# Optimization experiments

Measured on AMD Instinct MI355X. Metric: run time of the kernel, lower is better.

## Reference

```python
import jax, jax.numpy as jnp
import numpy as np

V, E, H, T, B = 32000, 1024, 1024, 128, 128


def setup_inputs() -> dict:
    key = jax.random.key(0)
    ks = jax.random.split(key, 12)
    inp = {
        "batch_a": jax.random.randint(ks[0], (T, B), 0, V),
        "batch_b": jax.random.randint(ks[1], (T, B), 0, V),
        "h0_a": jax.random.normal(ks[2], (B, H), jnp.float32),
        "c0_a": jax.random.normal(ks[3], (B, H), jnp.float32),
        "h0_b": jax.random.normal(ks[4], (B, H), jnp.float32),
        "c0_b": jax.random.normal(ks[5], (B, H), jnp.float32),
    }
    # shared encoder parameters (encoder_a and encoder_b are the same weights)
    emb = jax.random.normal(ks[6], (V, E), jnp.float32) * 0.02
    emb = emb.at[0].set(0.0)  # padding_idx=0
    scale = 1.0 / np.sqrt(H)
    inp["emb"] = emb
    inp["w_ih"] = jax.random.uniform(ks[7], (4 * H, E), jnp.float32, -scale, scale)
    inp["w_hh"] = jax.random.uniform(ks[8], (4 * H, H), jnp.float32, -scale, scale)
    b_ih = jax.random.uniform(ks[9], (4 * H,), jnp.float32, -scale, scale)
    b_hh = jax.random.uniform(ks[10], (4 * H,), jnp.float32, -scale, scale)
    # forget-gate bias filled with 2.5 (initialize_parameters fills [H:2H])
    inp["b_ih"] = b_ih.at[H:2 * H].set(2.5)
    inp["b_hh"] = b_hh.at[H:2 * H].set(2.5)
    return inp


def _lstm_final_hidden(ids, h0, c0, emb, w_ih, w_hh, b):
    # ids: [T, B]; returns final hidden state [B, H]
    x_seq = emb[ids]  # [T, B, E]

    def step(carry, x):
        h, c = carry
        gates = x @ w_ih.T + h @ w_hh.T + b  # [B, 4H]
        i, f, g, o = jnp.split(gates, 4, axis=-1)  # PyTorch gate order i,f,g,o
        c_new = jax.nn.sigmoid(f) * c + jax.nn.sigmoid(i) * jnp.tanh(g)
        h_new = jax.nn.sigmoid(o) * jnp.tanh(c_new)
        return (h_new, c_new), None

    (h_fin, _), _ = jax.lax.scan(step, (h0, c0), x_seq)
    return h_fin


def reference(batch_a, batch_b, h0_a, c0_a, h0_b, c0_b, emb, w_ih, w_hh, b_ih, b_hh):
    b = b_ih + b_hh
    enc_a = _lstm_final_hidden(batch_a, h0_a, c0_a, emb, w_ih, w_hh, b)
    enc_b = _lstm_final_hidden(batch_b, h0_b, c0_b, emb, w_ih, w_hh, b)
    # similarity: exp(-L1 distance per batch row)
    prediction = jnp.exp(-jnp.sum(jnp.abs(enc_a - enc_b), axis=1))  # [B]
    return prediction
```

## Files before the change

### kernel.cpp

```cpp
#include <hip/hip_runtime.h>


typedef unsigned char u8;
typedef unsigned short u16;
typedef unsigned long long u64;
typedef __attribute__((ext_vector_type(2))) unsigned long long u64x2;
typedef __attribute__((ext_vector_type(4))) float f32x4;

__device__ __forceinline__ u8 f2e4m3(float f) {
  unsigned ui = __builtin_bit_cast(unsigned, f);
  unsigned s = (ui >> 24) & 0x80u;
  float a = fabsf(f);
  if (a >= 448.f) return (u8)(s | 0x7Eu);
  if (a < 0.015625f) {
    int m = (int)rintf(a * 512.f);
    return (u8)(s | (unsigned)m);
  }
  unsigned au = ui & 0x7fffffffu;
  int e = (int)(au >> 23) - 127;
  float mm = __builtin_bit_cast(float, (au & 0x007fffffu) | 0x3f800000u);
  int q = (int)rintf((mm - 1.0f) * 8.0f);
  unsigned body = (unsigned)(((e + 7) << 3) + q);
  if (body > 0x7Eu) body = 0x7Eu;
  return (u8)(s | body);
}
__device__ __forceinline__ float e4m32f(u8 b) {
  unsigned e = (b >> 3) & 15u;
  unsigned m = b & 7u;
  float mag = (e == 0) ? (float)m * 0.001953125f
                       : __builtin_bit_cast(float, (e + 117u) << 23) * (float)(8u + m);
  return (b & 0x80u) ? -mag : mag;
}

__global__ __launch_bounds__(256) void prep_wf_kernel(const float* __restrict__ w_ih,
                                                      const float* __restrict__ w_hh,
                                                      u8* __restrict__ Wf) {
  unsigned idx = blockIdx.x * 256u + threadIdx.x;
  unsigned l = idx & 63u;
  unsigned kcg = (idx >> 6) & 63u;
  unsigned f = (idx >> 12) & 3u;
  unsigned nh = idx >> 14;
  unsigned r = f * 1024u + nh * 16u + (l & 15u);
  unsigned k0 = kcg * 32u + ((l >> 4) << 3);
  const float* src = (k0 < 1024u) ? (w_ih + (size_t)r * 1024u + k0)
                                  : (w_hh + (size_t)r * 1024u + (k0 - 1024u));
  float4 v0 = *(const float4*)src;
  float4 v1 = *(const float4*)(src + 4);
  u64 o = 0;
  o |= (u64)f2e4m3(v0.x * 16.f);
  o |= (u64)f2e4m3(v0.y * 16.f) << 8;
  o |= (u64)f2e4m3(v0.z * 16.f) << 16;
  o |= (u64)f2e4m3(v0.w * 16.f) << 24;
  o |= (u64)f2e4m3(v1.x * 16.f) << 32;
  o |= (u64)f2e4m3(v1.y * 16.f) << 40;
  o |= (u64)f2e4m3(v1.z * 16.f) << 48;
  o |= (u64)f2e4m3(v1.w * 16.f) << 56;
  *(u64*)(Wf + (size_t)idx * 8u) = o;
}

__global__ __launch_bounds__(256) void prep_state_kernel(
    const float* __restrict__ h0a, const float* __restrict__ h0b,
    const float* __restrict__ c0a, const float* __restrict__ c0b,
    const float* __restrict__ b_ih, const float* __restrict__ b_hh,
    const int* __restrict__ batch_a, const int* __restrict__ batch_b,
    const float* __restrict__ emb,
    float* __restrict__ bias, u8* __restrict__ hb0, float* __restrict__ cb,
    u8* __restrict__ xb0) {
  unsigned i = blockIdx.x * 256u + threadIdx.x;
  unsigned r = i >> 10;
  unsigned k = i & 1023u;
  float hv = (r < 128u) ? h0a[i] : h0b[i - 131072u];
  float cv = (r < 128u) ? c0a[i] : c0b[i - 131072u];
  hb0[i] = f2e4m3(hv);
  cb[i] = cv;
  int token = (r < 128u) ? batch_a[r] : batch_b[r - 128u];
  xb0[i] = f2e4m3(emb[(size_t)token * 1024u + k] * 16.f);
  if (i < 4096u) bias[i] = b_ih[i] + b_hh[i];
}

__global__ __launch_bounds__(512) void lstm_step_kernel(
    const int* __restrict__ batch_a, const int* __restrict__ batch_b,
    const float* __restrict__ emb, const u8* __restrict__ Wf,
    const float* __restrict__ bias,
    const u8* __restrict__ x_in, u8* __restrict__ x_next,
    const u8* __restrict__ h_in, u8* __restrict__ h_out,
    float* __restrict__ cbuf, int t) {
  __shared__ u8 As[2][2][64][128];
  __shared__ float Gs[2][64][68];

  const int tid = threadIdx.x;
  const int lane = tid & 63;
  const int w = tid >> 6;
  const int wm = (w >> 1) & 1, wn = w & 1, kg = w >> 2;
  const int m = blockIdx.x >> 6;
  const int nh = blockIdx.x & 63;

  f32x4 g0 = {0.f, 0.f, 0.f, 0.f}, g1 = {0.f, 0.f, 0.f, 0.f};
  const bool do_g = (t + 1 < 128) && (tid < 128);
  if (do_g) {
    int r = blockIdx.x;
    int token = (r < 128) ? batch_a[(t + 1) * 128 + r]
                          : batch_b[(t + 1) * 128 + (r - 128)];
    const f32x4* es = (const f32x4*)(emb + (size_t)token * 1024 + tid * 8);
    g0 = __builtin_nontemporal_load(es);
    g1 = __builtin_nontemporal_load(es + 1);
  }

  const int gtid = tid & 255;
  const int srow = gtid >> 2;
  const int q32 = (gtid & 3) << 5;
  const int wswz = (srow & 15) << 3;
  char* dstA0 = (char*)&As[kg][0][0][0] + srow * 128;
  char* dstA1 = (char*)&As[kg][1][0][0] + srow * 128;
  const u8* aBase = (kg == 0 ? x_in : h_in)
                    + ((size_t)(m * 64 + srow) << 10) + q32;

  const u8* wf0 = Wf + ((((size_t)(nh * 4 + wn * 2) * 64) + kg * 32) << 9) + lane * 8;
  const u8* wf1 = wf0 + (64 << 9);

  const int fr = lane & 15;
  const int fkb = (lane >> 4) << 3;
  const int Ra0 = wm * 32 + fr;
  const int Ra1 = Ra0 + 16;
  const int rswz = fr << 3;
  const char* A0 = (const char*)&As[kg][0][0][0];
  const char* A1 = (const char*)&As[kg][1][0][0];

  f32x4 acc[2][2];
#pragma unroll
  for (int a_ = 0; a_ < 2; ++a_)
#pragma unroll
    for (int b_ = 0; b_ < 2; ++b_) acc[a_][b_] = (f32x4){0.f, 0.f, 0.f, 0.f};

  u64x2 av0, av1;
  u64 brc[8], brn[8];
  av0 = *(const u64x2*)(aBase);
  av1 = *(const u64x2*)(aBase + 16);
#pragma unroll
  for (int kcl = 0; kcl < 4; ++kcl) {
    brc[kcl * 2]     = *(const u64*)(wf0 + (kcl << 9));
    brc[kcl * 2 + 1] = *(const u64*)(wf1 + (kcl << 9));
  }

#pragma unroll
  for (int it = 0; it < 8; ++it) {
    {
      char* dst = (it & 1) ? dstA1 : dstA0;
      *(u64*)(dst + ((q32 + 0)  ^ wswz)) = av0[0];
      *(u64*)(dst + ((q32 + 8)  ^ wswz)) = av0[1];
      *(u64*)(dst + ((q32 + 16) ^ wswz)) = av1[0];
      *(u64*)(dst + ((q32 + 24) ^ wswz)) = av1[1];
    }
    __syncthreads();
    if (it < 7) {
      const u8* an = aBase + (it + 1) * 128;
      av0 = *(const u64x2*)(an);
      av1 = *(const u64x2*)(an + 16);
#pragma unroll
      for (int kcl = 0; kcl < 4; ++kcl) {
        brn[kcl * 2]     = *(const u64*)(wf0 + (((it + 1) * 4 + kcl) << 9));
        brn[kcl * 2 + 1] = *(const u64*)(wf1 + (((it + 1) * 4 + kcl) << 9));
      }
    }
    const char* ab = (it & 1) ? A1 : A0;
#pragma unroll
    for (int kcl = 0; kcl < 4; ++kcl) {
      u64 af0 = *(const u64*)(ab + Ra0 * 128 + ((kcl * 32 + fkb) ^ rswz));
      u64 af1 = *(const u64*)(ab + Ra1 * 128 + ((kcl * 32 + fkb) ^ rswz));
      long a0 = __builtin_bit_cast(long, af0);
      long a1 = __builtin_bit_cast(long, af1);
      long b0 = __builtin_bit_cast(long, brc[kcl * 2]);
      long b1 = __builtin_bit_cast(long, brc[kcl * 2 + 1]);
      acc[0][0] = __builtin_amdgcn_mfma_f32_16x16x32_fp8_fp8(a0, b0, acc[0][0], 0, 0, 0);
      acc[0][1] = __builtin_amdgcn_mfma_f32_16x16x32_fp8_fp8(a0, b1, acc[0][1], 0, 0, 0);
      acc[1][0] = __builtin_amdgcn_mfma_f32_16x16x32_fp8_fp8(a1, b0, acc[1][0], 0, 0, 0);
      acc[1][1] = __builtin_amdgcn_mfma_f32_16x16x32_fp8_fp8(a1, b1, acc[1][1], 0, 0, 0);
    }
    if (it < 7) {
#pragma unroll
      for (int p = 0; p < 8; ++p) brc[p] = brn[p];
    }
  }

#pragma unroll
  for (int a_ = 0; a_ < 2; ++a_)
#pragma unroll
    for (int b_ = 0; b_ < 2; ++b_)
#pragma unroll
      for (int r_ = 0; r_ < 4; ++r_)
        Gs[kg][wm * 32 + a_ * 16 + ((lane >> 4) << 2) + r_][wn * 32 + b_ * 16 + fr] =
            acc[a_][b_][r_];
  __syncthreads();

  {
    const int crow = tid >> 3;
    const int u0 = (tid & 7) << 1;
    const int R2 = m * 64 + crow;
    const int gj = nh * 16 + u0;
    u8 hb8[2];
#pragma unroll
    for (int uu = 0; uu < 2; ++uu) {
      int cix = u0 + uu;
      int gjc = gj + uu;
      float iv = Gs[0][crow][cix]      * 0.00390625f + Gs[1][crow][cix]      * 0.0625f + bias[gjc];
      float fv = Gs[0][crow][16 + cix] * 0.00390625f + Gs[1][crow][16 + cix] * 0.0625f + bias[1024 + gjc];
      float gv = Gs[0][crow][32 + cix] * 0.00390625f + Gs[1][crow][32 + cix] * 0.0625f + bias[2048 + gjc];
      float ov = Gs[0][crow][48 + cix] * 0.00390625f + Gs[1][crow][48 + cix] * 0.0625f + bias[3072 + gjc];
      size_t ci = (size_t)R2 * 1024 + gjc;
      float c_old = cbuf[ci];
      float si = 1.f / (1.f + __expf(-iv));
      float sf = 1.f / (1.f + __expf(-fv));
      float so = 1.f / (1.f + __expf(-ov));
      float cn = sf * c_old + si * tanhf(gv);
      float hn = so * tanhf(cn);
      cbuf[ci] = cn;
      hb8[uu] = f2e4m3(hn);
    }
    u16 pk = (u16)hb8[0] | ((u16)hb8[1] << 8);
    *(u16*)(h_out + (size_t)R2 * 1024 + gj) = pk;
  }

  if (do_g) {
    int r = blockIdx.x;
    u64 o = 0;
    o |= (u64)f2e4m3(g0[0] * 16.f);
    o |= (u64)f2e4m3(g0[1] * 16.f) << 8;
    o |= (u64)f2e4m3(g0[2] * 16.f) << 16;
    o |= (u64)f2e4m3(g0[3] * 16.f) << 24;
    o |= (u64)f2e4m3(g1[0] * 16.f) << 32;
    o |= (u64)f2e4m3(g1[1] * 16.f) << 40;
    o |= (u64)f2e4m3(g1[2] * 16.f) << 48;
    o |= (u64)f2e4m3(g1[3] * 16.f) << 56;
    *(u64*)(x_next + (size_t)r * 1024 + tid * 8) = o;
  }
}

__global__ __launch_bounds__(256) void finalize_kernel(const u8* __restrict__ h,
                                                       float* __restrict__ out) {
  int b = blockIdx.x;
  int tid = threadIdx.x;
  const u8* ha = h + (size_t)b * 1024;
  const u8* hb = h + (size_t)(b + 128) * 1024;
  float s = 0.f;
  for (int j = tid; j < 1024; j += 256) s += fabsf(e4m32f(ha[j]) - e4m32f(hb[j]));
  __shared__ float red[256];
  red[tid] = s;
  __syncthreads();
  for (int off = 128; off > 0; off >>= 1) {
    if (tid < off) red[tid] += red[tid + off];
    __syncthreads();
  }
  if (tid == 0) out[b] = expf(-red[0]);
}

extern "C" void kernel_launch(void* const* d_in, const int* in_sizes, int n_in,
                              void* d_out, int out_size, void* d_ws, size_t ws_size,
                              hipStream_t stream) {
  const int* batch_a = (const int*)d_in[0];
  const int* batch_b = (const int*)d_in[1];
  const float* h0_a = (const float*)d_in[2];
  const float* c0_a = (const float*)d_in[3];
  const float* h0_b = (const float*)d_in[4];
  const float* c0_b = (const float*)d_in[5];
  const float* emb  = (const float*)d_in[6];
  const float* w_ih = (const float*)d_in[7];
  const float* w_hh = (const float*)d_in[8];
  const float* b_ih = (const float*)d_in[9];
  const float* b_hh = (const float*)d_in[10];

  char* ws = (char*)d_ws;
  u8*    Wf   = (u8*)(ws);
  float* bias = (float*)(ws + 8388608);
  u8*    xb0  = (u8*)(ws + 8404992);
  u8*    xb1  = (u8*)(ws + 8667136);
  u8*    hb0  = (u8*)(ws + 8929280);
  u8*    hb1  = (u8*)(ws + 9191424);
  float* cb   = (float*)(ws + 9453568);

  prep_wf_kernel<<<4096, 256, 0, stream>>>(w_ih, w_hh, Wf);
  prep_state_kernel<<<1024, 256, 0, stream>>>(h0_a, h0_b, c0_a, c0_b, b_ih, b_hh,
                                              batch_a, batch_b, emb, bias, hb0, cb, xb0);
  u8* xb[2] = {xb0, xb1};
  u8* hb[2] = {hb0, hb1};
  for (int t = 0; t < 128; ++t) {
    lstm_step_kernel<<<256, 512, 0, stream>>>(batch_a, batch_b, emb, Wf, bias,
                                              xb[t & 1], xb[(t + 1) & 1],
                                              hb[t & 1], hb[(t + 1) & 1], cb, t);
  }
  finalize_kernel<<<128, 256, 0, stream>>>(hb[0], (float*)d_out);
}
```

Baseline: 1.362 ms.

## Halve LSTM step block to 256 threads with four M-fragments per warp

The per-step LSTM kernel now runs 256 threads (4 warps) instead of 512. Each warp covers all 64 rows with four 16-row MFMA fragments instead of two, so every B-operand register is reused across twice as many MFMAs and the weight stream is loaded once per block rather than twice. The A-tile staging, the epilogue (now 4 hidden units per thread with vectorized c, bias and h stores) and the embedding prefetch are redistributed to fit the smaller block. In exchange each wave does twice the MFMA work and holds more accumulator registers, and fewer waves are left to hide latency in this latency-bound recurrent step.

```diff
diff --git a/kernel.cpp b/kernel.cpp
--- a/kernel.cpp
+++ b/kernel.cpp
@@ -78,7 +78,7 @@
   if (i < 4096u) bias[i] = b_ih[i] + b_hh[i];
 }
 
-__global__ __launch_bounds__(512) void lstm_step_kernel(
+__global__ __launch_bounds__(256) void lstm_step_kernel(
     const int* __restrict__ batch_a, const int* __restrict__ batch_b,
     const float* __restrict__ emb, const u8* __restrict__ Wf,
     const float* __restrict__ bias,
@@ -91,51 +91,49 @@
   const int tid = threadIdx.x;
   const int lane = tid & 63;
   const int w = tid >> 6;
-  const int wm = (w >> 1) & 1, wn = w & 1, kg = w >> 2;
+  const int kg = w >> 1, wn = w & 1;
   const int m = blockIdx.x >> 6;
   const int nh = blockIdx.x & 63;
 
-  f32x4 g0 = {0.f, 0.f, 0.f, 0.f}, g1 = {0.f, 0.f, 0.f, 0.f};
-  const bool do_g = (t + 1 < 128) && (tid < 128);
+  f32x4 g0 = {0.f, 0.f, 0.f, 0.f};
+  const bool do_g = (t + 1 < 128);
   if (do_g) {
     int r = blockIdx.x;
     int token = (r < 128) ? batch_a[(t + 1) * 128 + r]
                           : batch_b[(t + 1) * 128 + (r - 128)];
-    const f32x4* es = (const f32x4*)(emb + (size_t)token * 1024 + tid * 8);
-    g0 = __builtin_nontemporal_load(es);
-    g1 = __builtin_nontemporal_load(es + 1);
-  }
-
-  const int gtid = tid & 255;
-  const int srow = gtid >> 2;
-  const int q32 = (gtid & 3) << 5;
+    g0 = __builtin_nontemporal_load(
+        (const f32x4*)(emb + (size_t)token * 1024 + tid * 4));
+  }
+
+  const int skg = tid >> 7;
+  const int gtid = tid & 127;
+  const int srow = gtid >> 1;
+  const int qb = (gtid & 1) << 6;
   const int wswz = (srow & 15) << 3;
-  char* dstA0 = (char*)&As[kg][0][0][0] + srow * 128;
-  char* dstA1 = (char*)&As[kg][1][0][0] + srow * 128;
-  const u8* aBase = (kg == 0 ? x_in : h_in)
-                    + ((size_t)(m * 64 + srow) << 10) + q32;
+  char* dstA0 = (char*)&As[skg][0][0][0] + srow * 128;
+  char* dstA1 = (char*)&As[skg][1][0][0] + srow * 128;
+  const u8* aBase = (skg == 0 ? x_in : h_in)
+                    + ((size_t)(m * 64 + srow) << 10) + qb;
 
   const u8* wf0 = Wf + ((((size_t)(nh * 4 + wn * 2) * 64) + kg * 32) << 9) + lane * 8;
   const u8* wf1 = wf0 + (64 << 9);
 
   const int fr = lane & 15;
   const int fkb = (lane >> 4) << 3;
-  const int Ra0 = wm * 32 + fr;
-  const int Ra1 = Ra0 + 16;
   const int rswz = fr << 3;
   const char* A0 = (const char*)&As[kg][0][0][0];
   const char* A1 = (const char*)&As[kg][1][0][0];
 
-  f32x4 acc[2][2];
-#pragma unroll
-  for (int a_ = 0; a_ < 2; ++a_)
+  f32x4 acc[4][2];
+#pragma unroll
+  for (int a_ = 0; a_ < 4; ++a_)
 #pragma unroll
     for (int b_ = 0; b_ < 2; ++b_) acc[a_][b_] = (f32x4){0.f, 0.f, 0.f, 0.f};
 
-  u64x2 av0, av1;
+  u64x2 av[4];
   u64 brc[8], brn[8];
-  av0 = *(const u64x2*)(aBase);
-  av1 = *(const u64x2*)(aBase + 16);
+#pragma unroll
+  for (int q = 0; q < 4; ++q) av[q] = *(const u64x2*)(aBase + q * 16);
 #pragma unroll
   for (int kcl = 0; kcl < 4; ++kcl) {
     brc[kcl * 2]     = *(const u64*)(wf0 + (kcl << 9));
@@ -146,16 +144,17 @@
   for (int it = 0; it < 8; ++it) {
     {
       char* dst = (it & 1) ? dstA1 : dstA0;
-      *(u64*)(dst + ((q32 + 0)  ^ wswz)) = av0[0];
-      *(u64*)(dst + ((q32 + 8)  ^ wswz)) = av0[1];
-      *(u64*)(dst + ((q32 + 16) ^ wswz)) = av1[0];
-      *(u64*)(dst + ((q32 + 24) ^ wswz)) = av1[1];
+#pragma unroll
+      for (int q = 0; q < 4; ++q) {
+        *(u64*)(dst + ((qb + q * 16)     ^ wswz)) = av[q][0];
+        *(u64*)(dst + ((qb + q * 16 + 8) ^ wswz)) = av[q][1];
+      }
     }
     __syncthreads();
     if (it < 7) {
       const u8* an = aBase + (it + 1) * 128;
-      av0 = *(const u64x2*)(an);
-      av1 = *(const u64x2*)(an + 16);
+#pragma unroll
+      for (int q = 0; q < 4; ++q) av[q] = *(const u64x2*)(an + q * 16);
 #pragma unroll
       for (int kcl = 0; kcl < 4; ++kcl) {
         brn[kcl * 2]     = *(const u64*)(wf0 + (((it + 1) * 4 + kcl) << 9));
@@ -165,16 +164,15 @@
     const char* ab = (it & 1) ? A1 : A0;
 #pragma unroll
     for (int kcl = 0; kcl < 4; ++kcl) {
-      u64 af0 = *(const u64*)(ab + Ra0 * 128 + ((kcl * 32 + fkb) ^ rswz));
-      u64 af1 = *(const u64*)(ab + Ra1 * 128 + ((kcl * 32 + fkb) ^ rswz));
-      long a0 = __builtin_bit_cast(long, af0);
-      long a1 = __builtin_bit_cast(long, af1);
       long b0 = __builtin_bit_cast(long, brc[kcl * 2]);
       long b1 = __builtin_bit_cast(long, brc[kcl * 2 + 1]);
-      acc[0][0] = __builtin_amdgcn_mfma_f32_16x16x32_fp8_fp8(a0, b0, acc[0][0], 0, 0, 0);
-      acc[0][1] = __builtin_amdgcn_mfma_f32_16x16x32_fp8_fp8(a0, b1, acc[0][1], 0, 0, 0);
-      acc[1][0] = __builtin_amdgcn_mfma_f32_16x16x32_fp8_fp8(a1, b0, acc[1][0], 0, 0, 0);
-      acc[1][1] = __builtin_amdgcn_mfma_f32_16x16x32_fp8_fp8(a1, b1, acc[1][1], 0, 0, 0);
+#pragma unroll
+      for (int frg = 0; frg < 4; ++frg) {
+        u64 afu = *(const u64*)(ab + (frg * 16 + fr) * 128 + ((kcl * 32 + fkb) ^ rswz));
+        long a0 = __builtin_bit_cast(long, afu);
+        acc[frg][0] = __builtin_amdgcn_mfma_f32_16x16x32_fp8_fp8(a0, b0, acc[frg][0], 0, 0, 0);
+        acc[frg][1] = __builtin_amdgcn_mfma_f32_16x16x32_fp8_fp8(a0, b1, acc[frg][1], 0, 0, 0);
+      }
     }
     if (it < 7) {
 #pragma unroll
@@ -182,56 +180,58 @@
     }
   }
 
-#pragma unroll
-  for (int a_ = 0; a_ < 2; ++a_)
-#pragma unroll
-    for (int b_ = 0; b_ < 2; ++b_)
-#pragma unroll
-      for (int r_ = 0; r_ < 4; ++r_)
-        Gs[kg][wm * 32 + a_ * 16 + ((lane >> 4) << 2) + r_][wn * 32 + b_ * 16 + fr] =
-            acc[a_][b_][r_];
+  {
+    const int hi4 = (lane >> 4) << 2;
+#pragma unroll
+    for (int frg = 0; frg < 4; ++frg)
+#pragma unroll
+      for (int fc = 0; fc < 2; ++fc)
+#pragma unroll
+        for (int r_ = 0; r_ < 4; ++r_)
+          Gs[kg][frg * 16 + hi4 + r_][(wn * 2 + fc) * 16 + fr] = acc[frg][fc][r_];
+  }
   __syncthreads();
 
   {
-    const int crow = tid >> 3;
-    const int u0 = (tid & 7) << 1;
+    const int crow = tid >> 2;
+    const int u0 = (tid & 3) << 2;
     const int R2 = m * 64 + crow;
     const int gj = nh * 16 + u0;
-    u8 hb8[2];
-#pragma unroll
-    for (int uu = 0; uu < 2; ++uu) {
+    size_t ci = (size_t)R2 * 1024 + gj;
+    f32x4 c_old = *(const f32x4*)(cbuf + ci);
+    f32x4 bi = *(const f32x4*)(bias + gj);
+    f32x4 bf = *(const f32x4*)(bias + 1024 + gj);
+    f32x4 bg = *(const f32x4*)(bias + 2048 + gj);
+    f32x4 bo = *(const f32x4*)(bias + 3072 + gj);
+    f32x4 cnv;
+    unsigned pk = 0;
+#pragma unroll
+    for (int uu = 0; uu < 4; ++uu) {
       int cix = u0 + uu;
-      int gjc = gj + uu;
-      float iv = Gs[0][crow][cix]      * 0.00390625f + Gs[1][crow][cix]      * 0.0625f + bias[gjc];
-      float fv = Gs[0][crow][16 + cix] * 0.00390625f + Gs[1][crow][16 + cix] * 0.0625f + bias[1024 + gjc];
-      float gv = Gs[0][crow][32 + cix] * 0.00390625f + Gs[1][crow][32 + cix] * 0.0625f + bias[2048 + gjc];
-      float ov = Gs[0][crow][48 + cix] * 0.00390625f + Gs[1][crow][48 + cix] * 0.0625f + bias[3072 + gjc];
-      size_t ci = (size_t)R2 * 1024 + gjc;
-      float c_old = cbuf[ci];
+      float iv = Gs[0][crow][cix]      * 0.00390625f + Gs[1][crow][cix]      * 0.0625f + bi[uu];
+      float fv = Gs[0][crow][16 + cix] * 0.00390625f + Gs[1][crow][16 + cix] * 0.0625f + bf[uu];
+      float gv = Gs[0][crow][32 + cix] * 0.00390625f + Gs[1][crow][32 + cix] * 0.0625f + bg[uu];
+      float ov = Gs[0][crow][48 + cix] * 0.00390625f + Gs[1][crow][48 + cix] * 0.0625f + bo[uu];
       float si = 1.f / (1.f + __expf(-iv));
       float sf = 1.f / (1.f + __expf(-fv));
       float so = 1.f / (1.f + __expf(-ov));
-      float cn = sf * c_old + si * tanhf(gv);
+      float cn = sf * c_old[uu] + si * tanhf(gv);
+      cnv[uu] = cn;
       float hn = so * tanhf(cn);
-      cbuf[ci] = cn;
-      hb8[uu] = f2e4m3(hn);
-    }
-    u16 pk = (u16)hb8[0] | ((u16)hb8[1] << 8);
-    *(u16*)(h_out + (size_t)R2 * 1024 + gj) = pk;
+      pk |= ((unsigned)f2e4m3(hn)) << (uu * 8);
+    }
+    *(f32x4*)(cbuf + ci) = cnv;
+    *(unsigned*)(h_out + ci) = pk;
   }
 
   if (do_g) {
     int r = blockIdx.x;
-    u64 o = 0;
-    o |= (u64)f2e4m3(g0[0] * 16.f);
-    o |= (u64)f2e4m3(g0[1] * 16.f) << 8;
-    o |= (u64)f2e4m3(g0[2] * 16.f) << 16;
-    o |= (u64)f2e4m3(g0[3] * 16.f) << 24;
-    o |= (u64)f2e4m3(g1[0] * 16.f) << 32;
-    o |= (u64)f2e4m3(g1[1] * 16.f) << 40;
-    o |= (u64)f2e4m3(g1[2] * 16.f) << 48;
-    o |= (u64)f2e4m3(g1[3] * 16.f) << 56;
-    *(u64*)(x_next + (size_t)r * 1024 + tid * 8) = o;
+    unsigned o = 0;
+    o |= (unsigned)f2e4m3(g0[0] * 16.f);
+    o |= (unsigned)f2e4m3(g0[1] * 16.f) << 8;
+    o |= (unsigned)f2e4m3(g0[2] * 16.f) << 16;
+    o |= (unsigned)f2e4m3(g0[3] * 16.f) << 24;
+    *(unsigned*)(x_next + (size_t)r * 1024 + tid * 4) = o;
   }
 }
 
@@ -283,7 +283,7 @@
   u8* xb[2] = {xb0, xb1};
   u8* hb[2] = {hb0, hb1};
   for (int t = 0; t < 128; ++t) {
-    lstm_step_kernel<<<256, 512, 0, stream>>>(batch_a, batch_b, emb, Wf, bias,
+    lstm_step_kernel<<<256, 256, 0, stream>>>(batch_a, batch_b, emb, Wf, bias,
                                               xb[t & 1], xb[(t + 1) & 1],
                                               hb[t & 1], hb[(t + 1) & 1], cb, t);
   }
```

Result: slower. 1.415 ms (+3.9%).
